# Performance work log

Measured on AMD Instinct MI355X. Metric: run time of the kernel, lower is better.

## Reference

```python
import jax, jax.numpy as jnp
import numpy as np
import math

N_HEAD = 16
N_FEAT = 1024
O_FEAT = 1024
D_K = N_FEAT // N_HEAD


def setup_inputs() -> dict:
    key = jax.random.key(0)
    ks = jax.random.split(key, 11)
    B, L, DIN = 4, 2048, 1024
    s_in = 1.0 / math.sqrt(DIN)
    s_f = 1.0 / math.sqrt(N_FEAT)
    return {
        "query": jax.random.normal(ks[0], (B, L, DIN), jnp.float32),
        "key": jax.random.normal(ks[1], (B, L, DIN), jnp.float32),
        "value": jax.random.normal(ks[2], (B, L, DIN), jnp.float32),
        "Wq": jax.random.uniform(ks[3], (DIN, N_FEAT), jnp.float32, -s_in, s_in),
        "bq": jax.random.uniform(ks[4], (N_FEAT,), jnp.float32, -s_in, s_in),
        "Wk": jax.random.uniform(ks[5], (DIN, N_FEAT), jnp.float32, -s_in, s_in),
        "bk": jax.random.uniform(ks[6], (N_FEAT,), jnp.float32, -s_in, s_in),
        "Wv": jax.random.uniform(ks[7], (DIN, N_FEAT), jnp.float32, -s_in, s_in),
        "bv": jax.random.uniform(ks[8], (N_FEAT,), jnp.float32, -s_in, s_in),
        "Wo": jax.random.uniform(ks[9], (N_FEAT, O_FEAT), jnp.float32, -s_f, s_f),
        "bo": jax.random.uniform(ks[10], (O_FEAT,), jnp.float32, -s_f, s_f),
    }


def reference(query, key, value, Wq, bq, Wk, bk, Wv, bv, Wo, bo):
    B = query.shape[0]
    # QKV projections -> [B, H, L, Dk]
    def proj(x, W, b):
        y = x @ W + b
        return y.reshape(B, -1, N_HEAD, D_K).transpose(0, 2, 1, 3)
    q = proj(query, Wq, bq)
    k = proj(key, Wk, bk)
    v = proj(value, Wv, bv)
    # naive attention: full [B,H,Lq,Lk] scores
    scores = jnp.einsum("bhqd,bhkd->bhqk", q, k) / math.sqrt(D_K)
    attn = jax.nn.softmax(scores, axis=-1)  # dropout_rate=0 -> identity
    x = jnp.einsum("bhqk,bhkd->bhqd", attn, v)
    x = x.transpose(0, 2, 1, 3).reshape(B, -1, N_FEAT)
    return x @ Wo + bo
```

## Files before the change

### kernel.cpp

```cpp
#include <hip/hip_runtime.h>
#include <hip/hip_bf16.h>

#define DM 1024
#define LQ 2048

typedef __attribute__((ext_vector_type(8))) short short8;
typedef __attribute__((ext_vector_type(4))) float floatx4;

#define MFMA16(a, b, c) __builtin_amdgcn_mfma_f32_16x16x32_bf16((a), (b), (c), 0, 0, 0)
#define BAR() __builtin_amdgcn_s_barrier()
#define FENCE() asm volatile("" ::: "memory")
#define VWAIT4() asm volatile("s_waitcnt vmcnt(4)" ::: "memory")
#define VWAIT0() asm volatile("s_waitcnt vmcnt(0)" ::: "memory")

__device__ __forceinline__ unsigned short f2b(float f) {
  union { float f; unsigned u; } x; x.f = f;
  unsigned u = x.u;
  unsigned r = (u + 0x7fffu + ((u >> 16) & 1u)) >> 16;
  return (unsigned short)r;
}

__device__ __forceinline__ unsigned cvt_pk(float lo, float hi) {
  unsigned r;
  asm("v_cvt_pk_bf16_f32 %0, %1, %2" : "=v"(r) : "v"(lo), "v"(hi));
  return r;
}
__device__ __forceinline__ uint4 pack16(float4 a, float4 b) {
  return make_uint4(cvt_pk(a.x, a.y), cvt_pk(a.z, a.w),
                    cvt_pk(b.x, b.y), cvt_pk(b.z, b.w));
}

__device__ __forceinline__ void gl_lds16(const void* g, void* l) {
  __builtin_amdgcn_global_load_lds(
      (const __attribute__((address_space(1))) void*)g,
      (__attribute__((address_space(3))) void*)l, 16, 0, 0);
}

__device__ __forceinline__ void xcd_tiles(int bx, int by, int* m0, int* n0) {
  int flat = bx + (by << 3);
  int xcd = flat & 7;
  int loc = flat >> 3;
  *m0 = (xcd * 8 + (loc >> 3)) * 128;
  *n0 = (loc & 7) * 128;
}

__global__ __launch_bounds__(256) void cvt3(
    const float* __restrict__ A0, const float* __restrict__ A1,
    const float* __restrict__ A2,
    unsigned short* __restrict__ O0, unsigned short* __restrict__ O1,
    unsigned short* __restrict__ O2) {
  const float* s = (blockIdx.z == 0) ? A0 : (blockIdx.z == 1) ? A1 : A2;
  unsigned short* d = (blockIdx.z == 0) ? O0 : (blockIdx.z == 1) ? O1 : O2;
  size_t i = ((size_t)blockIdx.x * 256 + threadIdx.x) * 8;
  float4 f0 = *(const float4*)(s + i);
  float4 f1 = *(const float4*)(s + i + 4);
  *(uint4*)(d + i) = pack16(f0, f1);
}

__global__ __launch_bounds__(256) void transpose_w4(
    const float* __restrict__ W0, const float* __restrict__ W1,
    const float* __restrict__ W2, const float* __restrict__ W3,
    unsigned short* __restrict__ T0, unsigned short* __restrict__ T1,
    unsigned short* __restrict__ T2, unsigned short* __restrict__ T3) {
  __shared__ unsigned short t[64][65];
  const float* src; unsigned short* dst;
  switch (blockIdx.z) {
    case 0: src = W0; dst = T0; break;
    case 1: src = W1; dst = T1; break;
    case 2: src = W2; dst = T2; break;
    default: src = W3; dst = T3; break;
  }
  const int x = threadIdx.x & 63;
  const int y4 = threadIdx.x >> 6;
  const int c0 = blockIdx.x * 64;
  const int r0 = blockIdx.y * 64;
#pragma unroll
  for (int i = 0; i < 16; ++i) {
    int r = y4 * 16 + i;
    t[r][x] = f2b(src[(size_t)(r0 + r) * 1024 + c0 + x]);
  }
  __syncthreads();
#pragma unroll
  for (int i = 0; i < 16; ++i) {
    int r = y4 * 16 + i;
    dst[(size_t)(c0 + r) * 1024 + r0 + x] = t[x][r];
  }
}


__global__ __launch_bounds__(256) void gemm_qkv(
    const unsigned short* __restrict__ Aq, const unsigned short* __restrict__ Ak,
    const unsigned short* __restrict__ Av,
    const unsigned short* __restrict__ BtQ, const unsigned short* __restrict__ BtK,
    const unsigned short* __restrict__ BtV,
    const float* __restrict__ bq, const float* __restrict__ bk,
    const float* __restrict__ bv,
    unsigned short* __restrict__ Qb, unsigned short* __restrict__ Kb,
    unsigned short* __restrict__ Vt) {
  const int K = 1024, N = 1024;
  __shared__ unsigned short As[2][128 * 32];
  __shared__ unsigned short Bs[2][128 * 32];
  const int z = blockIdx.z;
  const unsigned short* A; const unsigned short* Bt; const float* bias;
  if (z == 0) { A = Aq; Bt = BtQ; bias = bq; }
  else if (z == 1) { A = Ak; Bt = BtK; bias = bk; }
  else { A = Av; Bt = BtV; bias = bv; }

  const int tid = threadIdx.x;
  const int wave = tid >> 6;
  const int lane = tid & 63;
  const int fm = lane & 15;
  const int quad = lane >> 4;
  int m0, n0;
  xcd_tiles(blockIdx.x, blockIdx.y, &m0, &n0);
  const int wm = (wave >> 1) * 64;
  const int wn = (wave & 1) * 64;

  floatx4 acc[4][4];
#pragma unroll
  for (int i = 0; i < 4; ++i)
#pragma unroll
    for (int j = 0; j < 4; ++j) acc[i][j] = (floatx4){0.f, 0.f, 0.f, 0.f};

  const int srow = lane >> 2;
  const int scol = (lane & 3) * 8;
  const unsigned short* Ag = A + (size_t)(m0 + wave * 32 + srow) * K + scol;
  const unsigned short* Bg = Bt + (size_t)(n0 + wave * 32 + srow) * K + scol;
  const int stA = wave * 32 * 32;

#pragma unroll
  for (int t = 0; t < 2; ++t) {
    gl_lds16(Ag + t * 32, &As[t][stA]);
    gl_lds16(Ag + t * 32 + (size_t)16 * K, &As[t][stA + 16 * 32]);
    gl_lds16(Bg + t * 32, &Bs[t][stA]);
    gl_lds16(Bg + t * 32 + (size_t)16 * K, &Bs[t][stA + 16 * 32]);
  }

#pragma unroll 1
  for (int t = 0; t < 30; ++t) {
    const int buf = t & 1;
    VWAIT4();
    BAR();
    FENCE();
    short8 a[4], b[4];
#pragma unroll
    for (int i = 0; i < 4; ++i)
      a[i] = *(const short8*)&As[buf][(wm + i * 16 + fm) * 32 + quad * 8];
#pragma unroll
    for (int j = 0; j < 4; ++j)
      b[j] = *(const short8*)&Bs[buf][(wn + j * 16 + fm) * 32 + quad * 8];
#pragma unroll
    for (int i = 0; i < 4; ++i)
#pragma unroll
      for (int j = 0; j < 4; ++j) acc[i][j] = MFMA16(a[i], b[j], acc[i][j]);
    BAR();
    FENCE();
    const int tn = t + 2;
    gl_lds16(Ag + tn * 32, &As[buf][stA]);
    gl_lds16(Ag + tn * 32 + (size_t)16 * K, &As[buf][stA + 16 * 32]);
    gl_lds16(Bg + tn * 32, &Bs[buf][stA]);
    gl_lds16(Bg + tn * 32 + (size_t)16 * K, &Bs[buf][stA + 16 * 32]);
  }
#pragma unroll
  for (int t = 30; t < 32; ++t) {
    if (t == 30) VWAIT4(); else VWAIT0();
    BAR();
    FENCE();
    const int buf = t & 1;
    short8 a[4], b[4];
#pragma unroll
    for (int i = 0; i < 4; ++i)
      a[i] = *(const short8*)&As[buf][(wm + i * 16 + fm) * 32 + quad * 8];
#pragma unroll
    for (int j = 0; j < 4; ++j)
      b[j] = *(const short8*)&Bs[buf][(wn + j * 16 + fm) * 32 + quad * 8];
#pragma unroll
    for (int i = 0; i < 4; ++i)
#pragma unroll
      for (int j = 0; j < 4; ++j) acc[i][j] = MFMA16(a[i], b[j], acc[i][j]);
  }

  float bvv[4];
#pragma unroll
  for (int j = 0; j < 4; ++j) bvv[j] = bias[n0 + wn + j * 16 + fm];

  if (z < 2) {
    const float sc = (z == 0) ? 0.1803368801111204f : 1.0f;
    unsigned short* C = (z == 0) ? Qb : Kb;
#pragma unroll
    for (int i = 0; i < 4; ++i) {
      int row = m0 + wm + i * 16 + quad * 4;
#pragma unroll
      for (int j = 0; j < 4; ++j) {
        int col = n0 + wn + j * 16 + fm;
#pragma unroll
        for (int r = 0; r < 4; ++r)
          C[(size_t)(row + r) * N + col] = f2b((acc[i][j][r] + bvv[j]) * sc);
      }
    }
  } else {
#pragma unroll
    for (int i = 0; i < 4; ++i) {
      int row = m0 + wm + i * 16 + quad * 4;
      int b = row >> 11, l = row & 2047;
#pragma unroll
      for (int j = 0; j < 4; ++j) {
        int col = n0 + wn + j * 16 + fm;
        int h = col >> 6, d = col & 63;
        uint2 pk;
        pk.x = cvt_pk(acc[i][j][0] + bvv[j], acc[i][j][1] + bvv[j]);
        pk.y = cvt_pk(acc[i][j][2] + bvv[j], acc[i][j][3] + bvv[j]);
        *(uint2*)&Vt[(((size_t)b * 16 + h) * 64 + d) * 2048 + l] = pk;
      }
    }
  }
}

__global__ __launch_bounds__(256) void gemm_bt_bias_f32(
    const unsigned short* __restrict__ A, const unsigned short* __restrict__ Bt,
    const float* __restrict__ bias, float* __restrict__ C,
    int M, int N, int K) {
  __shared__ unsigned short As[2][128 * 32];
  __shared__ unsigned short Bs[2][128 * 32];
  const int tid = threadIdx.x;
  const int wave = tid >> 6;
  const int lane = tid & 63;
  const int fm = lane & 15;
  const int quad = lane >> 4;
  int m0, n0;
  xcd_tiles(blockIdx.x, blockIdx.y, &m0, &n0);
  const int wm = (wave >> 1) * 64;
  const int wn = (wave & 1) * 64;

  floatx4 acc[4][4];
#pragma unroll
  for (int i = 0; i < 4; ++i)
#pragma unroll
    for (int j = 0; j < 4; ++j) acc[i][j] = (floatx4){0.f, 0.f, 0.f, 0.f};

  const int srow = lane >> 2;
  const int scol = (lane & 3) * 8;
  const unsigned short* Ag = A + (size_t)(m0 + wave * 32 + srow) * K + scol;
  const unsigned short* Bg = Bt + (size_t)(n0 + wave * 32 + srow) * K + scol;
  const int stA = wave * 32 * 32;

#pragma unroll
  for (int t = 0; t < 2; ++t) {
    gl_lds16(Ag + t * 32, &As[t][stA]);
    gl_lds16(Ag + t * 32 + (size_t)16 * K, &As[t][stA + 16 * 32]);
    gl_lds16(Bg + t * 32, &Bs[t][stA]);
    gl_lds16(Bg + t * 32 + (size_t)16 * K, &Bs[t][stA + 16 * 32]);
  }

#pragma unroll 1
  for (int t = 0; t < 30; ++t) {
    const int buf = t & 1;
    VWAIT4();
    BAR();
    FENCE();
    short8 a[4], b[4];
#pragma unroll
    for (int i = 0; i < 4; ++i)
      a[i] = *(const short8*)&As[buf][(wm + i * 16 + fm) * 32 + quad * 8];
#pragma unroll
    for (int j = 0; j < 4; ++j)
      b[j] = *(const short8*)&Bs[buf][(wn + j * 16 + fm) * 32 + quad * 8];
#pragma unroll
    for (int i = 0; i < 4; ++i)
#pragma unroll
      for (int j = 0; j < 4; ++j) acc[i][j] = MFMA16(a[i], b[j], acc[i][j]);
    BAR();
    FENCE();
    const int tn = t + 2;
    gl_lds16(Ag + tn * 32, &As[buf][stA]);
    gl_lds16(Ag + tn * 32 + (size_t)16 * K, &As[buf][stA + 16 * 32]);
    gl_lds16(Bg + tn * 32, &Bs[buf][stA]);
    gl_lds16(Bg + tn * 32 + (size_t)16 * K, &Bs[buf][stA + 16 * 32]);
  }
#pragma unroll
  for (int t = 30; t < 32; ++t) {
    if (t == 30) VWAIT4(); else VWAIT0();
    BAR();
    FENCE();
    const int buf = t & 1;
    short8 a[4], b[4];
#pragma unroll
    for (int i = 0; i < 4; ++i)
      a[i] = *(const short8*)&As[buf][(wm + i * 16 + fm) * 32 + quad * 8];
#pragma unroll
    for (int j = 0; j < 4; ++j)
      b[j] = *(const short8*)&Bs[buf][(wn + j * 16 + fm) * 32 + quad * 8];
#pragma unroll
    for (int i = 0; i < 4; ++i)
#pragma unroll
      for (int j = 0; j < 4; ++j) acc[i][j] = MFMA16(a[i], b[j], acc[i][j]);
  }

  float bv[4];
#pragma unroll
  for (int j = 0; j < 4; ++j) bv[j] = bias[n0 + wn + j * 16 + fm];
#pragma unroll
  for (int i = 0; i < 4; ++i) {
    int row = m0 + wm + i * 16 + quad * 4;
#pragma unroll
    for (int j = 0; j < 4; ++j) {
      int col = n0 + wn + j * 16 + fm;
#pragma unroll
      for (int r = 0; r < 4; ++r)
        C[(size_t)(row + r) * N + col] = acc[i][j][r] + bv[j];
    }
  }
}

__global__ __launch_bounds__(256, 4) void attn_kernel(
    const unsigned short* Qb, const unsigned short* __restrict__ Kb,
    const unsigned short* __restrict__ Vtg, unsigned short* Xb) {
  __shared__ unsigned short Ks[64 * 72];
  __shared__ unsigned short Vts[64 * 72];
  __shared__ unsigned short Ps[4 * 32 * 72];
  unsigned short* Qs = Ps;

  const int tid = threadIdx.x;
  const int wave = tid >> 6;
  const int lane = tid & 63;
  const int fm = lane & 15;
  const int quad = lane >> 4;
  const int qt = blockIdx.x;
  const int bh = blockIdx.y;
  const size_t base = (size_t)(bh >> 4) * (LQ * DM) + (size_t)(bh & 15) * 64;
  const unsigned short* Vg = Vtg + (size_t)bh * 64 * 2048;
  const int q0 = qt * 128;

#pragma unroll
  for (int it = 0; it < 4; ++it) {
    int idx = it * 256 + tid;
    int r = idx >> 3;
    int cc = (idx & 7) * 8;
    *(short8*)&Qs[r * 72 + cc] =
        *(const short8*)(Qb + base + (size_t)(q0 + r) * DM + cc);
  }
  __syncthreads();
  short8 qf[2][2];
#pragma unroll
  for (int mt = 0; mt < 2; ++mt)
#pragma unroll
    for (int ks = 0; ks < 2; ++ks)
      qf[mt][ks] = *(const short8*)&Qs[(wave * 32 + mt * 16 + fm) * 72 + ks * 32 + quad * 8];
  __syncthreads();

  short8 ones;
#pragma unroll
  for (int i = 0; i < 8; ++i) ones[i] = (short)0x3F80;

  floatx4 lacc[2];
  lacc[0] = (floatx4){0.f, 0.f, 0.f, 0.f};
  lacc[1] = (floatx4){0.f, 0.f, 0.f, 0.f};
  floatx4 oacc[4][2];
#pragma unroll
  for (int dt = 0; dt < 4; ++dt)
#pragma unroll
    for (int mt = 0; mt < 2; ++mt) oacc[dt][mt] = (floatx4){0.f, 0.f, 0.f, 0.f};

  unsigned short* Pw = &Ps[wave * 32 * 72];

  const int srow0 = tid >> 3;
  const int scc = (tid & 7) * 8;
  short8 kr[2], vr[2];
#pragma unroll
  for (int it = 0; it < 2; ++it) {
    int row = it * 32 + srow0;
    kr[it] = *(const short8*)(Kb + base + (size_t)row * DM + scc);
    vr[it] = *(const short8*)(Vg + (size_t)row * 2048 + scc);
  }

  for (int kt = 0; kt < 32; ++kt) {
    __syncthreads();
#pragma unroll
    for (int it = 0; it < 2; ++it) {
      int row = it * 32 + srow0;
      *(short8*)&Ks[row * 72 + scc] = kr[it];
      *(short8*)&Vts[row * 72 + scc] = vr[it];
    }
    __syncthreads();
    if (kt < 31) {
      int k0n = (kt + 1) * 64;
#pragma unroll
      for (int it = 0; it < 2; ++it) {
        int row = it * 32 + srow0;
        kr[it] = *(const short8*)(Kb + base + (size_t)(k0n + row) * DM + scc);
        vr[it] = *(const short8*)(Vg + (size_t)row * 2048 + k0n + scc);
      }
    }

    floatx4 sacc[4][2];
#pragma unroll
    for (int jt = 0; jt < 4; ++jt)
#pragma unroll
      for (int mt = 0; mt < 2; ++mt) sacc[jt][mt] = (floatx4){0.f, 0.f, 0.f, 0.f};
#pragma unroll
    for (int jt = 0; jt < 4; ++jt) {
      short8 k0f = *(const short8*)&Ks[(jt * 16 + fm) * 72 + quad * 8];
      short8 k1f = *(const short8*)&Ks[(jt * 16 + fm) * 72 + 32 + quad * 8];
#pragma unroll
      for (int mt = 0; mt < 2; ++mt) {
        sacc[jt][mt] = MFMA16(k0f, qf[mt][0], sacc[jt][mt]);
        sacc[jt][mt] = MFMA16(k1f, qf[mt][1], sacc[jt][mt]);
      }
    }

#pragma unroll
    for (int mt = 0; mt < 2; ++mt) {
      int rowoff = (mt * 16 + fm) * 72;
#pragma unroll
      for (int jt = 0; jt < 4; ++jt) {
        float p0 = __builtin_amdgcn_exp2f(sacc[jt][mt][0]);
        float p1 = __builtin_amdgcn_exp2f(sacc[jt][mt][1]);
        float p2 = __builtin_amdgcn_exp2f(sacc[jt][mt][2]);
        float p3 = __builtin_amdgcn_exp2f(sacc[jt][mt][3]);
        uint2 pk;
        pk.x = cvt_pk(p0, p1);
        pk.y = cvt_pk(p2, p3);
        *(uint2*)&Pw[rowoff + jt * 16 + quad * 4] = pk;
      }
    }

    __threadfence_block();

#pragma unroll
    for (int ks = 0; ks < 2; ++ks) {
      short8 pf0 = *(const short8*)&Pw[fm * 72 + ks * 32 + quad * 8];
      short8 pf1 = *(const short8*)&Pw[(16 + fm) * 72 + ks * 32 + quad * 8];
      lacc[0] = MFMA16(ones, pf0, lacc[0]);
      lacc[1] = MFMA16(ones, pf1, lacc[1]);
#pragma unroll
      for (int dt = 0; dt < 4; ++dt) {
        short8 vf = *(const short8*)&Vts[(dt * 16 + fm) * 72 + ks * 32 + quad * 8];
        oacc[dt][0] = MFMA16(vf, pf0, oacc[dt][0]);
        oacc[dt][1] = MFMA16(vf, pf1, oacc[dt][1]);
      }
    }
  }

  float inv[2];
  inv[0] = 1.0f / lacc[0][0];
  inv[1] = 1.0f / lacc[1][0];

#pragma unroll
  for (int mt = 0; mt < 2; ++mt) {
    int q = q0 + wave * 32 + mt * 16 + fm;
#pragma unroll
    for (int dt = 0; dt < 4; ++dt) {
      uint2 o;
      o.x = cvt_pk(oacc[dt][mt][0] * inv[mt], oacc[dt][mt][1] * inv[mt]);
      o.y = cvt_pk(oacc[dt][mt][2] * inv[mt], oacc[dt][mt][3] * inv[mt]);
      *(uint2*)&Xb[base + (size_t)q * DM + dt * 16 + quad * 4] = o;
    }
  }
}

extern "C" void kernel_launch(void* const* d_in, const int* in_sizes, int n_in,
                              void* d_out, int out_size, void* d_ws, size_t ws_size,
                              hipStream_t stream) {
  const float* q_in = (const float*)d_in[0];
  const float* k_in = (const float*)d_in[1];
  const float* v_in = (const float*)d_in[2];
  const float* Wq = (const float*)d_in[3];
  const float* bq = (const float*)d_in[4];
  const float* Wk = (const float*)d_in[5];
  const float* bk = (const float*)d_in[6];
  const float* Wv = (const float*)d_in[7];
  const float* bv = (const float*)d_in[8];
  const float* Wo = (const float*)d_in[9];
  const float* bo = (const float*)d_in[10];
  float* out = (float*)d_out;

  char* w = (char*)d_ws;
  unsigned short* WqT = (unsigned short*)w; w += 1024 * 1024 * 2;
  unsigned short* WkT = (unsigned short*)w; w += 1024 * 1024 * 2;
  unsigned short* WvT = (unsigned short*)w; w += 1024 * 1024 * 2;
  unsigned short* WoT = (unsigned short*)w; w += 1024 * 1024 * 2;
  unsigned short* Qb  = (unsigned short*)w; w += (size_t)8192 * 1024 * 2;
  unsigned short* Kb  = (unsigned short*)w; w += (size_t)8192 * 1024 * 2;
  unsigned short* Vt  = (unsigned short*)w; w += (size_t)8192 * 1024 * 2;
  unsigned short* Qa  = (unsigned short*)w; w += (size_t)8192 * 1024 * 2;
  unsigned short* Ka  = (unsigned short*)w; w += (size_t)8192 * 1024 * 2;
  unsigned short* Va  = (unsigned short*)w; w += (size_t)8192 * 1024 * 2;
  unsigned short* Xb  = Qb;

  transpose_w4<<<dim3(16, 16, 4), 256, 0, stream>>>(Wq, Wk, Wv, Wo,
                                                    WqT, WkT, WvT, WoT);

  cvt3<<<dim3(4096, 1, 3), 256, 0, stream>>>(q_in, k_in, v_in, Qa, Ka, Va);

  gemm_qkv<<<dim3(8, 64, 3), 256, 0, stream>>>(
      Qa, Ka, Va, WqT, WkT, WvT, bq, bk, bv, Qb, Kb, Vt);

  attn_kernel<<<dim3(16, 64), 256, 0, stream>>>(Qb, Kb, Vt, Xb);

  gemm_bt_bias_f32<<<dim3(8, 64), 256, 0, stream>>>(Xb, WoT, bo, out, 8192, 1024, 1024);
}
```

Before: 352.5 us.

## Halve attention query tile, shrink LDS/registers, raise occupancy, remap block order

The attention kernel now gives each block 64 query rows instead of 128 (16 per wave) and launches twice as many blocks. K, V and P share one smaller LDS buffer, and P is staged in two 32-column halves so it needs less space. Launch bounds go from 4 to 6 blocks per CU, and the block index is remapped so neighbouring blocks cover different batch-heads. The goal is more resident waves to hide latency and better cache locality. The cost is that each block loads K/V tiles for half as many queries, which doubles K/V global and LDS traffic per query, and the P handoff now needs two fences per K tile.

```diff
diff --git a/kernel.cpp b/kernel.cpp
--- a/kernel.cpp
+++ b/kernel.cpp
@@ -312,56 +312,47 @@
   }
 }
 
-__global__ __launch_bounds__(256, 4) void attn_kernel(
+__global__ __launch_bounds__(256, 6) void attn_kernel(
     const unsigned short* Qb, const unsigned short* __restrict__ Kb,
     const unsigned short* __restrict__ Vtg, unsigned short* Xb) {
-  __shared__ unsigned short Ks[64 * 72];
-  __shared__ unsigned short Vts[64 * 72];
-  __shared__ unsigned short Ps[4 * 32 * 72];
-  unsigned short* Qs = Ps;
-
+  __shared__ unsigned short lds[11776];
   const int tid = threadIdx.x;
   const int wave = tid >> 6;
   const int lane = tid & 63;
   const int fm = lane & 15;
   const int quad = lane >> 4;
-  const int qt = blockIdx.x;
-  const int bh = blockIdx.y;
+  const int flat = blockIdx.x + (blockIdx.y << 5);
+  const int qt = (flat >> 3) & 31;
+  const int bh = ((flat & 7) << 3) | (flat >> 8);
   const size_t base = (size_t)(bh >> 4) * (LQ * DM) + (size_t)(bh & 15) * 64;
   const unsigned short* Vg = Vtg + (size_t)bh * 64 * 2048;
-  const int q0 = qt * 128;
-
-#pragma unroll
-  for (int it = 0; it < 4; ++it) {
+  const int q0 = qt * 64;
+
+#pragma unroll
+  for (int it = 0; it < 2; ++it) {
     int idx = it * 256 + tid;
     int r = idx >> 3;
     int cc = (idx & 7) * 8;
-    *(short8*)&Qs[r * 72 + cc] =
+    *(short8*)&lds[r * 72 + cc] =
         *(const short8*)(Qb + base + (size_t)(q0 + r) * DM + cc);
   }
   __syncthreads();
-  short8 qf[2][2];
-#pragma unroll
-  for (int mt = 0; mt < 2; ++mt)
-#pragma unroll
-    for (int ks = 0; ks < 2; ++ks)
-      qf[mt][ks] = *(const short8*)&Qs[(wave * 32 + mt * 16 + fm) * 72 + ks * 32 + quad * 8];
+  short8 qf[2];
+#pragma unroll
+  for (int ks = 0; ks < 2; ++ks)
+    qf[ks] = *(const short8*)&lds[(wave * 16 + fm) * 72 + ks * 32 + quad * 8];
   __syncthreads();
 
   short8 ones;
 #pragma unroll
   for (int i = 0; i < 8; ++i) ones[i] = (short)0x3F80;
 
-  floatx4 lacc[2];
-  lacc[0] = (floatx4){0.f, 0.f, 0.f, 0.f};
-  lacc[1] = (floatx4){0.f, 0.f, 0.f, 0.f};
-  floatx4 oacc[4][2];
-#pragma unroll
-  for (int dt = 0; dt < 4; ++dt)
-#pragma unroll
-    for (int mt = 0; mt < 2; ++mt) oacc[dt][mt] = (floatx4){0.f, 0.f, 0.f, 0.f};
-
-  unsigned short* Pw = &Ps[wave * 32 * 72];
+  floatx4 lacc = (floatx4){0.f, 0.f, 0.f, 0.f};
+  floatx4 oacc[4];
+#pragma unroll
+  for (int dt = 0; dt < 4; ++dt) oacc[dt] = (floatx4){0.f, 0.f, 0.f, 0.f};
+
+  unsigned short* Pw = &lds[9216 + wave * 640];
 
   const int srow0 = tid >> 3;
   const int scc = (tid & 7) * 8;
@@ -378,8 +369,8 @@
 #pragma unroll
     for (int it = 0; it < 2; ++it) {
       int row = it * 32 + srow0;
-      *(short8*)&Ks[row * 72 + scc] = kr[it];
-      *(short8*)&Vts[row * 72 + scc] = vr[it];
+      *(short8*)&lds[row * 72 + scc] = kr[it];
+      *(short8*)&lds[4608 + row * 72 + scc] = vr[it];
     }
     __syncthreads();
     if (kt < 31) {
@@ -392,69 +383,53 @@
       }
     }
 
-    floatx4 sacc[4][2];
-#pragma unroll
-    for (int jt = 0; jt < 4; ++jt)
-#pragma unroll
-      for (int mt = 0; mt < 2; ++mt) sacc[jt][mt] = (floatx4){0.f, 0.f, 0.f, 0.f};
+    floatx4 sacc[4];
+#pragma unroll
+    for (int jt = 0; jt < 4; ++jt) sacc[jt] = (floatx4){0.f, 0.f, 0.f, 0.f};
 #pragma unroll
     for (int jt = 0; jt < 4; ++jt) {
-      short8 k0f = *(const short8*)&Ks[(jt * 16 + fm) * 72 + quad * 8];
-      short8 k1f = *(const short8*)&Ks[(jt * 16 + fm) * 72 + 32 + quad * 8];
-#pragma unroll
-      for (int mt = 0; mt < 2; ++mt) {
-        sacc[jt][mt] = MFMA16(k0f, qf[mt][0], sacc[jt][mt]);
-        sacc[jt][mt] = MFMA16(k1f, qf[mt][1], sacc[jt][mt]);
-      }
-    }
-
-#pragma unroll
-    for (int mt = 0; mt < 2; ++mt) {
-      int rowoff = (mt * 16 + fm) * 72;
-#pragma unroll
-      for (int jt = 0; jt < 4; ++jt) {
-        float p0 = __builtin_amdgcn_exp2f(sacc[jt][mt][0]);
-        float p1 = __builtin_amdgcn_exp2f(sacc[jt][mt][1]);
-        float p2 = __builtin_amdgcn_exp2f(sacc[jt][mt][2]);
-        float p3 = __builtin_amdgcn_exp2f(sacc[jt][mt][3]);
+      short8 k0f = *(const short8*)&lds[(jt * 16 + fm) * 72 + quad * 8];
+      short8 k1f = *(const short8*)&lds[(jt * 16 + fm) * 72 + 32 + quad * 8];
+      sacc[jt] = MFMA16(k0f, qf[0], sacc[jt]);
+      sacc[jt] = MFMA16(k1f, qf[1], sacc[jt]);
+    }
+
+#pragma unroll
+    for (int h = 0; h < 2; ++h) {
+      int rowoff = fm * 40;
+#pragma unroll
+      for (int jl = 0; jl < 2; ++jl) {
+        int jt = h * 2 + jl;
+        float p0 = __builtin_amdgcn_exp2f(sacc[jt][0]);
+        float p1 = __builtin_amdgcn_exp2f(sacc[jt][1]);
+        float p2 = __builtin_amdgcn_exp2f(sacc[jt][2]);
+        float p3 = __builtin_amdgcn_exp2f(sacc[jt][3]);
         uint2 pk;
         pk.x = cvt_pk(p0, p1);
         pk.y = cvt_pk(p2, p3);
-        *(uint2*)&Pw[rowoff + jt * 16 + quad * 4] = pk;
+        *(uint2*)&Pw[rowoff + jl * 16 + quad * 4] = pk;
       }
-    }
-
-    __threadfence_block();
-
-#pragma unroll
-    for (int ks = 0; ks < 2; ++ks) {
-      short8 pf0 = *(const short8*)&Pw[fm * 72 + ks * 32 + quad * 8];
-      short8 pf1 = *(const short8*)&Pw[(16 + fm) * 72 + ks * 32 + quad * 8];
-      lacc[0] = MFMA16(ones, pf0, lacc[0]);
-      lacc[1] = MFMA16(ones, pf1, lacc[1]);
+      __threadfence_block();
+      short8 pf = *(const short8*)&Pw[fm * 40 + quad * 8];
+      lacc = MFMA16(ones, pf, lacc);
 #pragma unroll
       for (int dt = 0; dt < 4; ++dt) {
-        short8 vf = *(const short8*)&Vts[(dt * 16 + fm) * 72 + ks * 32 + quad * 8];
-        oacc[dt][0] = MFMA16(vf, pf0, oacc[dt][0]);
-        oacc[dt][1] = MFMA16(vf, pf1, oacc[dt][1]);
+        short8 vf = *(const short8*)&lds[4608 + (dt * 16 + fm) * 72 + h * 32 + quad * 8];
+        oacc[dt] = MFMA16(vf, pf, oacc[dt]);
       }
-    }
-  }
-
-  float inv[2];
-  inv[0] = 1.0f / lacc[0][0];
-  inv[1] = 1.0f / lacc[1][0];
-
-#pragma unroll
-  for (int mt = 0; mt < 2; ++mt) {
-    int q = q0 + wave * 32 + mt * 16 + fm;
-#pragma unroll
-    for (int dt = 0; dt < 4; ++dt) {
-      uint2 o;
-      o.x = cvt_pk(oacc[dt][mt][0] * inv[mt], oacc[dt][mt][1] * inv[mt]);
-      o.y = cvt_pk(oacc[dt][mt][2] * inv[mt], oacc[dt][mt][3] * inv[mt]);
-      *(uint2*)&Xb[base + (size_t)q * DM + dt * 16 + quad * 4] = o;
-    }
+      FENCE();
+    }
+  }
+
+  float inv = 1.0f / lacc[0];
+
+  int q = q0 + wave * 16 + fm;
+#pragma unroll
+  for (int dt = 0; dt < 4; ++dt) {
+    uint2 o;
+    o.x = cvt_pk(oacc[dt][0] * inv, oacc[dt][1] * inv);
+    o.y = cvt_pk(oacc[dt][2] * inv, oacc[dt][3] * inv);
+    *(uint2*)&Xb[base + (size_t)q * DM + dt * 16 + quad * 4] = o;
   }
 }
 
@@ -495,7 +470,7 @@
   gemm_qkv<<<dim3(8, 64, 3), 256, 0, stream>>>(
       Qa, Ka, Va, WqT, WkT, WvT, bq, bk, bv, Qb, Kb, Vt);
 
-  attn_kernel<<<dim3(16, 64), 256, 0, stream>>>(Qb, Kb, Vt, Xb);
+  attn_kernel<<<dim3(32, 64), 256, 0, stream>>>(Qb, Kb, Vt, Xb);
 
   gemm_bt_bias_f32<<<dim3(8, 64), 256, 0, stream>>>(Xb, WoT, bo, out, 8192, 1024, 1024);
 }
```

New measurement: 382.3 us. 1.08x slower.
